# Kernel tuning notes

Hardware: AMD Instinct MI355X
Metric: run time of the kernel (lower is better)

Reference implementation:

```python
import jax, jax.numpy as jnp
import numpy as np

N = 40000
E = 640000
D_IN = 128
H = 8
C = 16  # out_dim per head


def setup_inputs() -> dict:
    key = jax.random.key(0)
    ks = jax.random.split(key, 7)
    features = jax.random.normal(ks[0], (N, D_IN), dtype=jnp.float32)
    edge_index = jax.random.randint(ks[1], (2, E), 0, N, dtype=jnp.int32)
    edge_weight = jax.random.uniform(ks[2], (E,), dtype=jnp.float32)
    # xavier-ish scales
    W_lin = jax.random.normal(ks[3], (D_IN, H * C), dtype=jnp.float32) * (1.0 / np.sqrt(D_IN))
    att_l = jax.random.normal(ks[4], (1, H, C), dtype=jnp.float32) * 0.1
    att_r = jax.random.normal(ks[5], (1, H, C), dtype=jnp.float32) * 0.1
    W_res = jax.random.normal(ks[6], (D_IN, H * C), dtype=jnp.float32) * (1.0 / np.sqrt(D_IN))
    return {"features": features, "edge_index": edge_index, "edge_weight": edge_weight,
            "W_lin": W_lin, "att_l": att_l, "att_r": att_r, "W_res": W_res}


def _segment_softmax(logits, seg, num_segments):
    # logits: (E, H), seg: (E,) destination node ids
    m = jax.ops.segment_max(logits, seg, num_segments=num_segments)  # (N, H)
    ex = jnp.exp(logits - m[seg])
    s = jax.ops.segment_sum(ex, seg, num_segments=num_segments)  # (N, H)
    return ex / s[seg]


def reference(features, edge_index, edge_weight, W_lin, att_l, att_r, W_res):
    src, dst = edge_index[0], edge_index[1]
    x = (features @ W_lin).reshape(-1, H, C)              # (N, H, C)
    alpha_l = (x * att_l).sum(-1)                          # (N, H)
    alpha_r = (x * att_r).sum(-1)                          # (N, H)
    alpha = alpha_l[src] + alpha_r[dst]                    # (E, H)
    alpha = edge_weight[:, None] * alpha
    alpha = jnp.where(alpha >= 0, alpha, 0.2 * alpha)      # leaky_relu(0.2)
    coef = _segment_softmax(alpha, dst, N)                 # (E, H)
    msgs = x[src] * coef[:, :, None]                       # (E, H, C)
    agg = jax.ops.segment_sum(msgs, dst, num_segments=N)   # (N, H, C)
    out = jax.nn.elu(agg).reshape(-1, H * C)
    out = out + features @ W_res
    return out
```

## Files before the change

kernel.cpp:

```cpp
#include <hip/hip_runtime.h>
#include <math.h>

#define N_NODES 40000
#define N_EDGES 640000
#define D 128
#define H 8
#define C 16
#define NBG 1250
#define KP 136
#define NBUCK 625
#define NCH 512
#define ECH 1250
#define CAP 12
#define SLOTS (NCH * CAP)
#define MAXB 1536
#define OVCAP 4096

typedef __attribute__((ext_vector_type(8))) short short8;
typedef __attribute__((ext_vector_type(4))) float floatx4;


__device__ __forceinline__ unsigned short f2bf(float f) {
  const unsigned u = __float_as_uint(f);
  return (unsigned short)((u + 0x7FFFu + ((u >> 16) & 1u)) >> 16);
}
__device__ __forceinline__ float bflo(unsigned p) {
  return __uint_as_float(p << 16);
}
__device__ __forceinline__ float bfhi(unsigned p) {
  return __uint_as_float(p & 0xFFFF0000u);
}
__device__ __forceinline__ float bf2f(unsigned short u) {
  return __uint_as_float((unsigned)u << 16);
}

__global__ void k_prep(const float* __restrict__ Wlin,
                       const float* __restrict__ Wres,
                       unsigned short* __restrict__ wt, int* __restrict__ ovfn)
{
  const int n = blockIdx.x, k = threadIdx.x, g = blockIdx.y;
  if (n == 0 && g == 0 && k == 0) *ovfn = 0;
  const float* W = g ? Wres : Wlin;
  wt[((g * 128 + n) * 128) + k] = f2bf(W[(long)k * 128 + n]);
}

__global__ __launch_bounds__(256, 4) void k_gemm(
    const float* __restrict__ feat, const unsigned short* __restrict__ wt,
    unsigned short* __restrict__ xh, float* __restrict__ outp,
    const float* __restrict__ attl, const float* __restrict__ attr,
    float* __restrict__ al, float* __restrict__ ar,
    const int* __restrict__ src, const int* __restrict__ dst,
    const float* __restrict__ ew, uint2* __restrict__ einfo,
    int* __restrict__ cnt2, int* __restrict__ ovfn, uint4* __restrict__ ovf)
{
  __shared__ short sA[32 * KP];
  __shared__ float sD[32 * 132];
  const int t = threadIdx.x;

  if (blockIdx.y == 1) {
    if (blockIdx.x >= NCH) return;
    int* lcnt = (int*)sA;
    for (int i = t; i < NBUCK; i += 256) lcnt[i] = 0;
    __syncthreads();
    const int c = blockIdx.x, e0 = c * ECH;
    for (int e = e0 + t; e < e0 + ECH; e += 256) {
      const int d = dst[e];
      const int b = d >> 6, dl = d & 63;
      const int r = atomicAdd(&lcnt[b], 1);
      const unsigned pay = ((unsigned)src[e] << 6) | (unsigned)dl;
      const unsigned wbits = __float_as_uint(ew[e]);
      if (r < CAP) {
        einfo[((long)b * NCH + c) * CAP + r] = make_uint2(pay, wbits);
      } else {
        const int oi = atomicAdd(ovfn, 1);
        if (oi < OVCAP)
          ovf[oi] = make_uint4((unsigned)b, (unsigned)dl,
                               (unsigned)src[e], wbits);
      }
    }
    __syncthreads();
    for (int i = t; i < NBUCK; i += 256) cnt2[c * NBUCK + i] = lcnt[i];
    return;
  }

  const int row0 = blockIdx.x * 32;

  {
    const int kq = t & 31;
    const int rb = (t >> 5) * 4;
    #pragma unroll
    for (int i = 0; i < 4; ++i) {
      const int r = rb + i;
      const float4 f = *(const float4*)&feat[(long)(row0 + r) * 128 + kq * 4];
      const unsigned lo = (unsigned)f2bf(f.x) | ((unsigned)f2bf(f.y) << 16);
      const unsigned hi = (unsigned)f2bf(f.z) | ((unsigned)f2bf(f.w) << 16);
      *(uint2*)&sA[r * KP + kq * 4] = make_uint2(lo, hi);
    }
  }

  const int w = t >> 6, lane = t & 63;
  const int c15 = lane & 15, q = lane >> 4;

  short8 bfr0[4][2], bfr1[4][2];
  #pragma unroll
  for (int kc = 0; kc < 4; ++kc)
    #pragma unroll
    for (int nt = 0; nt < 2; ++nt) {
      const int n = (w * 2 + nt) * 16 + c15;
      bfr0[kc][nt] = *(const short8*)&wt[n * 128 + kc * 32 + q * 8];
      bfr1[kc][nt] = *(const short8*)&wt[16384 + n * 128 + kc * 32 + q * 8];
    }
  __syncthreads();

  floatx4 acc0[2][2], acc1[2][2];
  #pragma unroll
  for (int mt = 0; mt < 2; ++mt)
    #pragma unroll
    for (int nt = 0; nt < 2; ++nt) {
      acc0[mt][nt] = (floatx4){0.f, 0.f, 0.f, 0.f};
      acc1[mt][nt] = (floatx4){0.f, 0.f, 0.f, 0.f};
    }
  #pragma unroll
  for (int kc = 0; kc < 4; ++kc)
    #pragma unroll
    for (int mt = 0; mt < 2; ++mt) {
      const short8 afr = *(const short8*)&sA[(mt * 16 + c15) * KP + kc * 32 + q * 8];
      acc0[mt][0] = __builtin_amdgcn_mfma_f32_16x16x32_bf16(afr, bfr0[kc][0], acc0[mt][0], 0, 0, 0);
      acc0[mt][1] = __builtin_amdgcn_mfma_f32_16x16x32_bf16(afr, bfr0[kc][1], acc0[mt][1], 0, 0, 0);
      acc1[mt][0] = __builtin_amdgcn_mfma_f32_16x16x32_bf16(afr, bfr1[kc][0], acc1[mt][0], 0, 0, 0);
      acc1[mt][1] = __builtin_amdgcn_mfma_f32_16x16x32_bf16(afr, bfr1[kc][1], acc1[mt][1], 0, 0, 0);
    }

  const int orow = t >> 3, seg = t & 7;
  const int grow = row0 + orow;

  #pragma unroll
  for (int mt = 0; mt < 2; ++mt)
    #pragma unroll
    for (int nt = 0; nt < 2; ++nt) {
      const int col = (w * 2 + nt) * 16 + c15;
      #pragma unroll
      for (int r = 0; r < 4; ++r)
        sD[(mt * 16 + q * 4 + r) * 132 + col] = acc0[mt][nt][r];
    }
  __syncthreads();
  {
    #pragma unroll
    for (int i = 0; i < 2; ++i) {
      const float4 v0 = *(const float4*)&sD[orow * 132 + seg * 16 + i * 8];
      const float4 v1 = *(const float4*)&sD[orow * 132 + seg * 16 + i * 8 + 4];
      uint4 u;
      u.x = (unsigned)f2bf(v0.x) | ((unsigned)f2bf(v0.y) << 16);
      u.y = (unsigned)f2bf(v0.z) | ((unsigned)f2bf(v0.w) << 16);
      u.z = (unsigned)f2bf(v1.x) | ((unsigned)f2bf(v1.y) << 16);
      u.w = (unsigned)f2bf(v1.z) | ((unsigned)f2bf(v1.w) << 16);
      *(uint4*)&xh[(long)grow * 128 + seg * 16 + i * 8] = u;
    }
    const int h = seg;
    float sl = 0.f, sr = 0.f;
    #pragma unroll
    for (int c4 = 0; c4 < 4; ++c4) {
      const float4 xv = *(const float4*)&sD[orow * 132 + h * 16 + c4 * 4];
      const float4 lv = *(const float4*)&attl[h * 16 + c4 * 4];
      const float4 rv = *(const float4*)&attr[h * 16 + c4 * 4];
      sl += xv.x * lv.x + xv.y * lv.y + xv.z * lv.z + xv.w * lv.w;
      sr += xv.x * rv.x + xv.y * rv.y + xv.z * rv.z + xv.w * rv.w;
    }
    al[(long)grow * 8 + h] = sl;
    ar[(long)grow * 8 + h] = sr;
  }
  __syncthreads();

  #pragma unroll
  for (int mt = 0; mt < 2; ++mt)
    #pragma unroll
    for (int nt = 0; nt < 2; ++nt) {
      const int col = (w * 2 + nt) * 16 + c15;
      #pragma unroll
      for (int r = 0; r < 4; ++r)
        sD[(mt * 16 + q * 4 + r) * 132 + col] = acc1[mt][nt][r];
    }
  __syncthreads();
  #pragma unroll
  for (int i = 0; i < 4; ++i) {
    const float4 v = *(const float4*)&sD[orow * 132 + seg * 16 + i * 4];
    *(float4*)&outp[(long)grow * 128 + seg * 16 + i * 4] = v;
  }
}

__global__ __launch_bounds__(1024, 4) void k_edgeagg(
    const int* __restrict__ cnt2, const uint2* __restrict__ einfo,
    const int* __restrict__ ovfn, const uint4* __restrict__ ovf,
    const float* __restrict__ al, const float* __restrict__ ar,
    const unsigned short* __restrict__ xh, float* __restrict__ outp)
{
  __shared__ uint2 sE[MAXB];
  __shared__ unsigned short sP[MAXB * 8];
  __shared__ int sS[MAXB];
  __shared__ float sAr[512];
  __shared__ int scnt[NCH];
  __shared__ int bcnt[64], bbase[64], bpos[64];
  __shared__ int nE;
  const int b = blockIdx.x;
  const int t = threadIdx.x;
  if (t < 64) bcnt[t] = 0;
  if (t == 64) nE = 0;
  if (t < 512) sAr[t] = ar[((long)(b << 6)) * 8 + t];
  else scnt[t - 512] = min(cnt2[(t - 512) * NBUCK + b], CAP);
  __syncthreads();

  const long base = (long)b * SLOTS;
  for (int i = t; i < SLOTS; i += 1024) {
    const int c = i / CAP;
    const int r = i - c * CAP;
    if (r < scnt[c]) {
      const uint2 m = einfo[base + i];
      const int k = atomicAdd(&nE, 1);
      sE[k] = m;
      atomicAdd(&bcnt[m.x & 63], 1);
    }
  }
  const int no = *ovfn;
  for (int i = t; i < no; i += 1024) {
    const uint4 o = ovf[i];
    if ((int)o.x == b) {
      const int k = atomicAdd(&nE, 1);
      sE[k] = make_uint2((o.z << 6) | o.y, o.w);
      atomicAdd(&bcnt[o.y], 1);
    }
  }
  __syncthreads();
  const int cntb = nE;

  if (t < 64) {
    const int v = bcnt[t];
    int incl = v;
    #pragma unroll
    for (int off = 1; off < 64; off <<= 1) {
      const int n = __shfl_up(incl, off, 64);
      if (t >= off) incl += n;
    }
    bbase[t] = incl - v;
    bpos[t] = 0;
  }
  __syncthreads();

  for (int i = t; i < cntb; i += 1024) {
    const uint2 m = sE[i];
    const int dl = m.x & 63;
    const int s = (int)(m.x >> 6);
    const float w = __uint_as_float(m.y);
    const float4 l0 = *(const float4*)&al[(long)s * 8];
    const float4 l1 = *(const float4*)&al[(long)s * 8 + 4];
    const float* arr = &sAr[dl * 8];
    float lv[8] = {l0.x + arr[0], l0.y + arr[1], l0.z + arr[2], l0.w + arr[3],
                   l1.x + arr[4], l1.y + arr[5], l1.z + arr[6], l1.w + arr[7]};
    #pragma unroll
    for (int h = 0; h < 8; ++h) {
      float a = w * lv[h];
      a = (a >= 0.f) ? a : 0.2f * a;
      lv[h] = __expf(a);
    }
    const int r = atomicAdd(&bpos[dl], 1);
    const int qq = bbase[dl] + r;
    sS[qq] = s;
    uint4 u;
    u.x = (unsigned)f2bf(lv[0]) | ((unsigned)f2bf(lv[1]) << 16);
    u.y = (unsigned)f2bf(lv[2]) | ((unsigned)f2bf(lv[3]) << 16);
    u.z = (unsigned)f2bf(lv[4]) | ((unsigned)f2bf(lv[5]) << 16);
    u.w = (unsigned)f2bf(lv[6]) | ((unsigned)f2bf(lv[7]) << 16);
    *(uint4*)&sP[qq * 8] = u;
  }
  __syncthreads();

  const int wv = t >> 6, lane = t & 63;
  const int h = lane >> 3;
  const int co = lane * 2;
  #pragma unroll
  for (int j = 0; j < 4; ++j) {
    const int dl = wv * 4 + j;
    const int start = bbase[dl];
    const int end = start + bcnt[dl];
    if (end <= start) continue;

    float2 a0 = {0.f, 0.f}, a1 = {0.f, 0.f}, a2 = {0.f, 0.f}, a3 = {0.f, 0.f};
    float s0s = 0.f, s1s = 0.f, s2s = 0.f, s3s = 0.f;
    int p = start;
    for (; p + 4 <= end; p += 4) {
      const int s0 = sS[p + 0], s1 = sS[p + 1];
      const int s2 = sS[p + 2], s3 = sS[p + 3];
      const float e0v = bf2f(sP[(p + 0) * 8 + h]);
      const float e1v = bf2f(sP[(p + 1) * 8 + h]);
      const float e2v = bf2f(sP[(p + 2) * 8 + h]);
      const float e3v = bf2f(sP[(p + 3) * 8 + h]);
      const unsigned v0 = *(const unsigned*)&xh[(long)s0 * 128 + co];
      const unsigned v1 = *(const unsigned*)&xh[(long)s1 * 128 + co];
      const unsigned v2 = *(const unsigned*)&xh[(long)s2 * 128 + co];
      const unsigned v3 = *(const unsigned*)&xh[(long)s3 * 128 + co];
      a0.x = fmaf(bflo(v0), e0v, a0.x); a0.y = fmaf(bfhi(v0), e0v, a0.y); s0s += e0v;
      a1.x = fmaf(bflo(v1), e1v, a1.x); a1.y = fmaf(bfhi(v1), e1v, a1.y); s1s += e1v;
      a2.x = fmaf(bflo(v2), e2v, a2.x); a2.y = fmaf(bfhi(v2), e2v, a2.y); s2s += e2v;
      a3.x = fmaf(bflo(v3), e3v, a3.x); a3.y = fmaf(bfhi(v3), e3v, a3.y); s3s += e3v;
    }
    for (; p < end; ++p) {
      const int s = sS[p];
      const float ev = bf2f(sP[p * 8 + h]);
      const unsigned v = *(const unsigned*)&xh[(long)s * 128 + co];
      a0.x = fmaf(bflo(v), ev, a0.x);
      a0.y = fmaf(bfhi(v), ev, a0.y);
      s0s += ev;
    }
    const float rs = 1.0f / ((s0s + s1s) + (s2s + s3s));
    const float ax = ((a0.x + a1.x) + (a2.x + a3.x)) * rs;
    const float ay = ((a0.y + a1.y) + (a2.y + a3.y)) * rs;

    const long dnode = (long)(b << 6) + dl;
    float2 o = *(float2*)&outp[dnode * 128 + co];
    o.x += (ax > 0.f) ? ax : expm1f(ax);
    o.y += (ay > 0.f) ? ay : expm1f(ay);
    *(float2*)&outp[dnode * 128 + co] = o;
  }
}

extern "C" void kernel_launch(void* const* d_in, const int* in_sizes, int n_in,
                              void* d_out, int out_size, void* d_ws, size_t ws_size,
                              hipStream_t stream) {
  const float* feat = (const float*)d_in[0];
  const int*   eidx = (const int*)d_in[1];
  const float* ew   = (const float*)d_in[2];
  const float* Wlin = (const float*)d_in[3];
  const float* attl = (const float*)d_in[4];
  const float* attr = (const float*)d_in[5];
  const float* Wres = (const float*)d_in[6];
  float* outp = (float*)d_out;

  float* ws = (float*)d_ws;
  unsigned short* xh = (unsigned short*)ws;
  float* al   = ws + 5120000;
  float* ar   = ws + 5440000;
  uint2* einfo = (uint2*)(ws + 6000000);
  int*   cnt2 = (int*)(ws + 14000000);
  int*   ovfn = (int*)(ws + 14400000);
  uint4* ovf  = (uint4*)(ws + 14400064);
  unsigned short* wt = (unsigned short*)(ws + 15000000);

  const int* src = eidx;
  const int* dst = eidx + N_EDGES;

  dim3 pgrid(128, 2);
  k_prep<<<pgrid, 128, 0, stream>>>(Wlin, Wres, wt, ovfn);
  dim3 ggrid(NBG, 2);
  k_gemm<<<ggrid, 256, 0, stream>>>(feat, wt, xh, outp, attl, attr, al, ar,
                                    src, dst, ew, einfo, cnt2, ovfn, ovf);
  k_edgeagg<<<NBUCK, 1024, 0, stream>>>(cnt2, einfo, ovfn, ovf, al, ar,
                                        xh, outp);
}
```

Baseline: 150.0 us.

## Use smaller 16-node destination buckets with 256-thread aggregation blocks

```diff
diff --git a/kernel.cpp b/kernel.cpp
--- a/kernel.cpp
+++ b/kernel.cpp
@@ -8,13 +8,14 @@
 #define C 16
 #define NBG 1250
 #define KP 136
-#define NBUCK 625
-#define NCH 512
-#define ECH 1250
-#define CAP 12
-#define SLOTS (NCH * CAP)
-#define MAXB 1536
+#define NBUCK 2500
+#define NCH 128
+#define ECH 5000
+#define CAP 8
+#define SLOTS_B (NCH * CAP)
+#define MAXB 384
 #define OVCAP 4096
+#define SOVC 64
 
 typedef __attribute__((ext_vector_type(8))) short short8;
 typedef __attribute__((ext_vector_type(4))) float floatx4;
@@ -59,15 +60,16 @@
 
   if (blockIdx.y == 1) {
     if (blockIdx.x >= NCH) return;
-    int* lcnt = (int*)sA;
+    int* lcnt = (int*)sD;
     for (int i = t; i < NBUCK; i += 256) lcnt[i] = 0;
     __syncthreads();
-    const int c = blockIdx.x, e0 = c * ECH;
+    const int c = blockIdx.x;
+    const int e0 = c * ECH;
     for (int e = e0 + t; e < e0 + ECH; e += 256) {
       const int d = dst[e];
-      const int b = d >> 6, dl = d & 63;
+      const int b = d >> 4, dl = d & 15;
       const int r = atomicAdd(&lcnt[b], 1);
-      const unsigned pay = ((unsigned)src[e] << 6) | (unsigned)dl;
+      const unsigned pay = ((unsigned)src[e] << 4) | (unsigned)dl;
       const unsigned wbits = __float_as_uint(ew[e]);
       if (r < CAP) {
         einfo[((long)b * NCH + c) * CAP + r] = make_uint2(pay, wbits);
@@ -188,56 +190,54 @@
   }
 }
 
-__global__ __launch_bounds__(1024, 4) void k_edgeagg(
+__global__ __launch_bounds__(256, 8) void k_edgeagg(
     const int* __restrict__ cnt2, const uint2* __restrict__ einfo,
     const int* __restrict__ ovfn, const uint4* __restrict__ ovf,
     const float* __restrict__ al, const float* __restrict__ ar,
     const unsigned short* __restrict__ xh, float* __restrict__ outp)
 {
-  __shared__ uint2 sE[MAXB];
   __shared__ unsigned short sP[MAXB * 8];
   __shared__ int sS[MAXB];
-  __shared__ float sAr[512];
+  __shared__ float sAr[128];
   __shared__ int scnt[NCH];
-  __shared__ int bcnt[64], bbase[64], bpos[64];
-  __shared__ int nE;
+  __shared__ uint2 sOv[SOVC];
+  __shared__ int bcnt[16], bbase[16], bpos[16], nOv;
   const int b = blockIdx.x;
   const int t = threadIdx.x;
-  if (t < 64) bcnt[t] = 0;
-  if (t == 64) nE = 0;
-  if (t < 512) sAr[t] = ar[((long)(b << 6)) * 8 + t];
-  else scnt[t - 512] = min(cnt2[(t - 512) * NBUCK + b], CAP);
-  __syncthreads();
-
-  const long base = (long)b * SLOTS;
-  for (int i = t; i < SLOTS; i += 1024) {
-    const int c = i / CAP;
-    const int r = i - c * CAP;
+  if (t < 16) bcnt[t] = 0;
+  if (t == 16) nOv = 0;
+  if (t < 128) sAr[t] = ar[(long)(b << 4) * 8 + t];
+  if (t >= 128) scnt[t - 128] = min(cnt2[(t - 128) * NBUCK + b], CAP);
+  __syncthreads();
+
+  const long base = (long)b * SLOTS_B;
+
+  for (int i = t; i < SLOTS_B; i += 256) {
+    const int c = i >> 3, r = i & 7;
     if (r < scnt[c]) {
       const uint2 m = einfo[base + i];
-      const int k = atomicAdd(&nE, 1);
-      sE[k] = m;
-      atomicAdd(&bcnt[m.x & 63], 1);
+      atomicAdd(&bcnt[m.x & 15], 1);
     }
   }
   const int no = *ovfn;
-  for (int i = t; i < no; i += 1024) {
+  for (int i = t; i < no; i += 256) {
     const uint4 o = ovf[i];
     if ((int)o.x == b) {
-      const int k = atomicAdd(&nE, 1);
-      sE[k] = make_uint2((o.z << 6) | o.y, o.w);
-      atomicAdd(&bcnt[o.y], 1);
-    }
-  }
-  __syncthreads();
-  const int cntb = nE;
-
-  if (t < 64) {
+      const int k = atomicAdd(&nOv, 1);
+      if (k < SOVC) {
+        sOv[k] = make_uint2((o.z << 4) | o.y, o.w);
+        atomicAdd(&bcnt[o.y], 1);
+      }
+    }
+  }
+  __syncthreads();
+
+  if (t < 16) {
     const int v = bcnt[t];
     int incl = v;
     #pragma unroll
-    for (int off = 1; off < 64; off <<= 1) {
-      const int n = __shfl_up(incl, off, 64);
+    for (int off = 1; off < 16; off <<= 1) {
+      const int n = __shfl_up(incl, off, 16);
       if (t >= off) incl += n;
     }
     bbase[t] = incl - v;
@@ -245,10 +245,9 @@
   }
   __syncthreads();
 
-  for (int i = t; i < cntb; i += 1024) {
-    const uint2 m = sE[i];
-    const int dl = m.x & 63;
-    const int s = (int)(m.x >> 6);
+  auto process = [&](uint2 m) {
+    const int dl = m.x & 15;
+    const int s = (int)(m.x >> 4);
     const float w = __uint_as_float(m.y);
     const float4 l0 = *(const float4*)&al[(long)s * 8];
     const float4 l1 = *(const float4*)&al[(long)s * 8 + 4];
@@ -270,7 +269,13 @@
     u.z = (unsigned)f2bf(lv[4]) | ((unsigned)f2bf(lv[5]) << 16);
     u.w = (unsigned)f2bf(lv[6]) | ((unsigned)f2bf(lv[7]) << 16);
     *(uint4*)&sP[qq * 8] = u;
-  }
+  };
+  for (int i = t; i < SLOTS_B; i += 256) {
+    const int c = i >> 3, r = i & 7;
+    if (r < scnt[c]) process(einfo[base + i]);
+  }
+  const int nov = min(nOv, SOVC);
+  for (int i = t; i < nov; i += 256) process(sOv[i]);
   __syncthreads();
 
   const int wv = t >> 6, lane = t & 63;
@@ -314,7 +319,7 @@
     const float ax = ((a0.x + a1.x) + (a2.x + a3.x)) * rs;
     const float ay = ((a0.y + a1.y) + (a2.y + a3.y)) * rs;
 
-    const long dnode = (long)(b << 6) + dl;
+    const long dnode = (long)(b << 4) + dl;
     float2 o = *(float2*)&outp[dnode * 128 + co];
     o.x += (ax > 0.f) ? ax : expm1f(ax);
     o.y += (ay > 0.f) ? ay : expm1f(ay);
@@ -339,10 +344,10 @@
   float* al   = ws + 5120000;
   float* ar   = ws + 5440000;
   uint2* einfo = (uint2*)(ws + 6000000);
-  int*   cnt2 = (int*)(ws + 14000000);
-  int*   ovfn = (int*)(ws + 14400000);
-  uint4* ovf  = (uint4*)(ws + 14400064);
-  unsigned short* wt = (unsigned short*)(ws + 15000000);
+  int*   cnt2 = (int*)(ws + 11500000);
+  int*   ovfn = (int*)(ws + 12000000);
+  uint4* ovf  = (uint4*)(ws + 12000064);
+  unsigned short* wt = (unsigned short*)(ws + 12800000);
 
   const int* src = eidx;
   const int* dst = eidx + N_EDGES;
@@ -352,6 +357,6 @@
   dim3 ggrid(NBG, 2);
   k_gemm<<<ggrid, 256, 0, stream>>>(feat, wt, xh, outp, attl, attr, al, ar,
                                     src, dst, ew, einfo, cnt2, ovfn, ovf);
-  k_edgeagg<<<NBUCK, 1024, 0, stream>>>(cnt2, einfo, ovfn, ovf, al, ar,
-                                        xh, outp);
-}
+  k_edgeagg<<<NBUCK, 256, 0, stream>>>(cnt2, einfo, ovfn, ovf, al, ar,
+                                       xh, outp);
+}
```

Result: slower. 171.6 us (+14.4%).
